# Performance work log

Measured on AMD Instinct MI355X. Metric: run time of the kernel, lower is better.

The kernel has to match this reference:

```python
import jax, jax.numpy as jnp
import numpy as np

B, C_IN, C_OUT = 16, 96, 192
N_IN, N_OUT, K = 16384, 4096, 16
SIGMA, MAX_ORD = 0.05, 2
M = 2 * MAX_ORD + 1  # basis size: 1 + cos/sin up to max_ord
BN_EPS = 1e-5


def _build_graph(rng):
    # random vertex layout; out vertices are a subset of in vertices
    vin = rng.standard_normal((N_IN, 2)).astype(np.float32)
    vout = vin[rng.choice(N_IN, N_OUT, replace=False)]
    idx = np.empty((N_OUT, K), np.int64)
    for s in range(0, N_OUT, 1024):  # chunked exact k-NN
        d = ((vout[s:s + 1024, None, :] - vin[None, :, :]) ** 2).sum(-1)
        idx[s:s + 1024] = np.argpartition(d, K, axis=1)[:, :K]
    rel = vin[idx] - vout[:, None, :]            # [N_out, K, 2]
    r2 = (rel ** 2).sum(-1)
    theta = np.arctan2(rel[..., 1], rel[..., 0])
    gauss = np.exp(-r2 / (2.0 * SIGMA ** 2))
    harm = [np.ones_like(theta)]
    for m in range(1, MAX_ORD + 1):
        harm += [np.cos(m * theta), np.sin(m * theta)]
    basis = (gauss[..., None] * np.stack(harm, -1)).astype(np.float32)  # [N_out, K, M]
    return idx, basis


def setup_inputs() -> dict:
    rng = np.random.default_rng(0)
    idx, basis = _build_graph(rng)
    key = jax.random.key(0)
    k0, k1, k2 = jax.random.split(key, 3)
    return {
        "x": jax.random.normal(k0, (B, C_IN, N_IN), jnp.float32),
        "idx": jnp.asarray(idx),
        "basis": jnp.asarray(basis),
        "conv_w": jax.random.normal(k1, (C_OUT, C_IN, M), jnp.float32) * 0.02,
        "conv_b": jnp.zeros((C_OUT,), jnp.float32),
        "pool_w": jax.random.normal(k2, (C_OUT, C_IN), jnp.float32) * 0.02,
        "pool_b": jnp.zeros((C_OUT,), jnp.float32),
        "gamma": jnp.ones((C_OUT,), jnp.float32),
        "beta": jnp.zeros((C_OUT,), jnp.float32),
    }


def reference(x, idx, basis, conv_w, conv_b, pool_w, pool_b, gamma, beta):
    # irregular k-NN gather: [B, C_in, N_out, K]
    neigh = x[:, :, idx]
    # identity path: AvgPool over k neighbors + 1x1 conv
    pooled = neigh.mean(axis=-1)                                   # [B, C_in, N_out]
    identity = jnp.einsum('oc,bcn->bon', pool_w, pooled) + pool_b[:, None]
    # ConvV2: project neighbors onto gaussian-harmonic basis, contract with weights
    feat = jnp.einsum('bcnk,nkm->bcnm', neigh, basis)              # [B, C_in, N_out, M]
    out = jnp.einsum('ocm,bcnm->bon', conv_w, feat) + conv_b[:, None]
    # BatchNorm1d (training-mode batch stats over B and N)
    mean = out.mean(axis=(0, 2), keepdims=True)
    var = out.var(axis=(0, 2), keepdims=True)
    out = (out - mean) * jax.lax.rsqrt(var + BN_EPS) * gamma[:, None] + beta[:, None]
    return out + identity
```

## Files before the change

kernel.cpp:

```cpp
#include <hip/hip_runtime.h>

typedef __attribute__((ext_vector_type(8))) short s16x8;
typedef __attribute__((ext_vector_type(4))) float f32x4;

constexpr int cB = 16, cCIN = 96, cCOUT = 192, cNIN = 16384, cNOUT = 4096;
constexpr float cEPS = 1e-5f;

constexpr size_t OFF_XT     = 0;
constexpr size_t OFF_CONVB  = 0;
constexpr size_t OFF_IDENTB = 25165824;
constexpr size_t OFF_FEATA  = 50331648;
constexpr size_t OFF_WB     = 125829120;
constexpr size_t OFF_SS     = 126050304;
constexpr size_t OFF_S1     = 126051840;
constexpr size_t OFF_S2     = 127624704;

__device__ inline unsigned bf16_rne(float f) {
    unsigned u = __builtin_bit_cast(unsigned, f);
    return (u + 0x7fffu + ((u >> 16) & 1u)) >> 16;
}
__device__ inline float bf16_f(unsigned short h) {
    unsigned u = ((unsigned)h) << 16;
    return __builtin_bit_cast(float, u);
}

__launch_bounds__(256)
__global__ void k_tr(const float* __restrict__ x, unsigned* __restrict__ xto) {
    __shared__ float s[96 * 133];
    const int b = blockIdx.y, j0 = blockIdx.x * 128, t = threadIdx.x;
    const float* xb = x + (size_t)b * 96 * 16384 + j0;
    for (int q = t; q < 3072; q += 256) {
        int c = q >> 5, j4 = (q & 31) * 4;
        float4 v = *(const float4*)(xb + (size_t)c * 16384 + j4);
        s[c * 133 + j4 + 0] = v.x;
        s[c * 133 + j4 + 1] = v.y;
        s[c * 133 + j4 + 2] = v.z;
        s[c * 133 + j4 + 3] = v.w;
    }
    __syncthreads();
    for (int q = t; q < 6144; q += 256) {
        int cp = q % 48, jj = q / 48;
        float f0 = s[(2 * cp) * 133 + jj];
        float f1 = s[(2 * cp + 1) * 133 + jj];
        unsigned pr = bf16_rne(f0) | (bf16_rne(f1) << 16);
        xto[(size_t)(b * 16384 + j0 + jj) * 48 + cp] = pr;
    }
}

__global__ void k_pack(const float* __restrict__ cw, const float* __restrict__ pw,
                       unsigned short* __restrict__ wB) {
    int e = blockIdx.x * 256 + threadIdx.x;
    if (e >= 110592) return;
    int r = e & 7, l = (e >> 3) & 63;
    int ts = e >> 9;
    int s = ts % 18, ot = ts / 18;
    int o = ot * 16 + (l & 15);
    int ko = s * 32 + ((l >> 4) << 3) + r;
    float v;
    if (ko < 480) { int m = ko / 96, c = ko % 96; v = cw[(o * 96 + c) * 5 + m]; }
    else          { int c = ko - 480;             v = pw[o * 96 + c]; }
    wB[e] = (unsigned short)bf16_rne(v);
}

__launch_bounds__(192)
__global__ void k_feat(const unsigned short* __restrict__ xt,
                       const int* __restrict__ idx,
                       const float* __restrict__ basis,
                       unsigned short* __restrict__ featA) {
    __shared__ float s_bas[16 * 97];
    __shared__ int s_idx[256];
    const int t = threadIdx.x, b = blockIdx.y, n0 = blockIdx.x * 16;

    for (int i = t; i < 256; i += 192)
        s_idx[i] = idx[n0 * 16 + i];
    for (int i = t; i < 16 * 96; i += 192) {
        int nl = i / 96, km = i % 96, k = km / 6, m = km % 6;
        float v = (m < 5) ? basis[((size_t)(n0 + nl) * 16 + k) * 5 + m] : 0.0625f;
        s_bas[nl * 97 + km] = v;
    }
    __syncthreads();

    const int c8 = t >> 4, nl = t & 15;
    float fm[6][8];
#pragma unroll
    for (int m = 0; m < 6; ++m)
#pragma unroll
        for (int j = 0; j < 8; ++j) fm[m][j] = 0.f;

    const size_t xbase = (size_t)b * 16384;
#pragma unroll 4
    for (int k = 0; k < 16; ++k) {
        int j = s_idx[nl * 16 + k];
        s16x8 v = *(const s16x8*)(xt + (xbase + j) * 96 + c8 * 8);
        float gf[8];
#pragma unroll
        for (int q = 0; q < 8; ++q) gf[q] = bf16_f((unsigned short)v[q]);
#pragma unroll
        for (int m = 0; m < 6; ++m) {
            float bv = s_bas[nl * 97 + k * 6 + m];
#pragma unroll
            for (int q = 0; q < 8; ++q) fm[m][q] = fmaf(gf[q], bv, fm[m][q]);
        }
    }

    const int tile = b * 256 + blockIdx.x;
    const int fl = nl + ((c8 & 3) << 4);
#pragma unroll
    for (int m = 0; m < 6; ++m) {
        int s = 3 * m + (c8 >> 2);
        uint4 o;
        o.x = bf16_rne(fm[m][0]) | (bf16_rne(fm[m][1]) << 16);
        o.y = bf16_rne(fm[m][2]) | (bf16_rne(fm[m][3]) << 16);
        o.z = bf16_rne(fm[m][4]) | (bf16_rne(fm[m][5]) << 16);
        o.w = bf16_rne(fm[m][6]) | (bf16_rne(fm[m][7]) << 16);
        *(uint4*)(featA + ((size_t)(tile * 18 + s) * 64 + fl) * 8) = o;
    }
}

__launch_bounds__(256)
__global__ void k_gemm(const unsigned short* __restrict__ featA,
                       const unsigned short* __restrict__ wB,
                       unsigned short* __restrict__ convb,
                       unsigned short* __restrict__ identb,
                       float* __restrict__ s1g,
                       float* __restrict__ s2g) {
    __shared__ __align__(16) unsigned short s_c[192 * 72];
    const int t = threadIdx.x;
    const int w = t >> 6, lane = t & 63;
    const int wr = w & 1, wc = w >> 1;
    const int bid = blockIdx.x;
    const int tile0 = bid * 4 + wr * 2;
    const s16x8* A  = (const s16x8*)featA;
    const s16x8* Bw = (const s16x8*)wB;

    f32x4 accC[2][6], accI[2][6];
    const f32x4 z = {0.f, 0.f, 0.f, 0.f};
#pragma unroll
    for (int rt = 0; rt < 2; ++rt)
#pragma unroll
        for (int j = 0; j < 6; ++j) { accC[rt][j] = z; accI[rt][j] = z; }

    for (int s = 0; s < 15; ++s) {
        s16x8 a0 = A[(size_t)(tile0 * 18 + s) * 64 + lane];
        s16x8 a1 = A[(size_t)((tile0 + 1) * 18 + s) * 64 + lane];
#pragma unroll
        for (int j = 0; j < 6; ++j) {
            s16x8 bf = Bw[(size_t)((wc * 6 + j) * 18 + s) * 64 + lane];
            accC[0][j] = __builtin_amdgcn_mfma_f32_16x16x32_bf16(a0, bf, accC[0][j], 0, 0, 0);
            accC[1][j] = __builtin_amdgcn_mfma_f32_16x16x32_bf16(a1, bf, accC[1][j], 0, 0, 0);
        }
    }
#pragma unroll
    for (int s = 15; s < 18; ++s) {
        s16x8 a0 = A[(size_t)(tile0 * 18 + s) * 64 + lane];
        s16x8 a1 = A[(size_t)((tile0 + 1) * 18 + s) * 64 + lane];
#pragma unroll
        for (int j = 0; j < 6; ++j) {
            s16x8 bf = Bw[(size_t)((wc * 6 + j) * 18 + s) * 64 + lane];
            accI[0][j] = __builtin_amdgcn_mfma_f32_16x16x32_bf16(a0, bf, accI[0][j], 0, 0, 0);
            accI[1][j] = __builtin_amdgcn_mfma_f32_16x16x32_bf16(a1, bf, accI[1][j], 0, 0, 0);
        }
    }

    const int col_l = lane & 15, rg = (lane >> 4) * 4;
    const int b  = (bid * 64) >> 12;
    const int n0 = (bid * 64) & 4095;

#pragma unroll
    for (int j = 0; j < 6; ++j) {
        float s1 = 0.f, s2 = 0.f;
#pragma unroll
        for (int rt = 0; rt < 2; ++rt)
#pragma unroll
            for (int r = 0; r < 4; ++r) {
                float v = accC[rt][j][r];
                s1 += v;
                s2 = fmaf(v, v, s2);
            }
        s1 += __shfl_xor(s1, 16); s2 += __shfl_xor(s2, 16);
        s1 += __shfl_xor(s1, 32); s2 += __shfl_xor(s2, 32);
        if (lane < 16) {
            int o = (wc * 6 + j) * 16 + lane;
            s1g[(size_t)o * 2048 + bid * 2 + wr] = s1;
            s2g[(size_t)o * 2048 + bid * 2 + wr] = s2;
        }
    }

#pragma unroll
    for (int rt = 0; rt < 2; ++rt) {
        int lr = (wr * 2 + rt) * 16 + rg;
#pragma unroll
        for (int j = 0; j < 6; ++j) {
            int o = (wc * 6 + j) * 16 + col_l;
#pragma unroll
            for (int r = 0; r < 4; ++r)
                s_c[o * 72 + lr + r] = (unsigned short)bf16_rne(accC[rt][j][r]);
        }
    }
    __syncthreads();
    for (int u = t; u < 1536; u += 256) {
        int o = u >> 3, part = u & 7;
        uint4 v = *(const uint4*)(&s_c[o * 72 + part * 8]);
        *(uint4*)(convb + ((size_t)(b * 192 + o)) * 4096 + n0 + part * 8) = v;
    }
    __syncthreads();
#pragma unroll
    for (int rt = 0; rt < 2; ++rt) {
        int lr = (wr * 2 + rt) * 16 + rg;
#pragma unroll
        for (int j = 0; j < 6; ++j) {
            int o = (wc * 6 + j) * 16 + col_l;
#pragma unroll
            for (int r = 0; r < 4; ++r)
                s_c[o * 72 + lr + r] = (unsigned short)bf16_rne(accI[rt][j][r]);
        }
    }
    __syncthreads();
    for (int u = t; u < 1536; u += 256) {
        int o = u >> 3, part = u & 7;
        uint4 v = *(const uint4*)(&s_c[o * 72 + part * 8]);
        *(uint4*)(identb + ((size_t)(b * 192 + o)) * 4096 + n0 + part * 8) = v;
    }
}

__launch_bounds__(256)
__global__ void k_ss(const float* __restrict__ s1g, const float* __restrict__ s2g,
                     const float* __restrict__ gamma, const float* __restrict__ beta,
                     const float* __restrict__ pool_b, float* __restrict__ ss) {
    int o = blockIdx.x, t = threadIdx.x;
    float s1 = 0.f, s2 = 0.f;
    for (int i = t; i < 2048; i += 256) {
        s1 += s1g[(size_t)o * 2048 + i];
        s2 += s2g[(size_t)o * 2048 + i];
    }
#pragma unroll
    for (int off = 32; off; off >>= 1) {
        s1 += __shfl_down(s1, off);
        s2 += __shfl_down(s2, off);
    }
    __shared__ float w1[4], w2[4];
    int lane = t & 63, wid = t >> 6;
    if (lane == 0) { w1[wid] = s1; w2[wid] = s2; }
    __syncthreads();
    if (t == 0) {
        float S1 = w1[0] + w1[1] + w1[2] + w1[3];
        float S2 = w2[0] + w2[1] + w2[2] + w2[3];
        float inv  = 1.0f / (cB * cNOUT);
        float mean = S1 * inv;
        float var  = S2 * inv - mean * mean;
        float scale = gamma[o] * rsqrtf(var + cEPS);
        ss[o]         = scale;
        ss[cCOUT + o] = beta[o] - mean * scale + pool_b[o];
    }
}

__launch_bounds__(256)
__global__ void k_final(const unsigned short* __restrict__ convb,
                        const unsigned short* __restrict__ identb,
                        const float* __restrict__ ss,
                        float* __restrict__ out) {
    size_t i = ((size_t)blockIdx.x * 256 + threadIdx.x) * 8;
    int o = (int)((i >> 12) % cCOUT);
    uint4 cv = *(const uint4*)(convb + i);
    uint4 dv = *(const uint4*)(identb + i);
    const unsigned short* ch = (const unsigned short*)&cv;
    const unsigned short* dh = (const unsigned short*)&dv;
    float sc = ss[o], sh = ss[cCOUT + o];
    float r[8];
#pragma unroll
    for (int j = 0; j < 8; ++j)
        r[j] = fmaf(bf16_f(ch[j]), sc, sh + bf16_f(dh[j]));
    *(float4*)(out + i)     = *(float4*)&r[0];
    *(float4*)(out + i + 4) = *(float4*)&r[4];
}

extern "C" void kernel_launch(void* const* d_in, const int* in_sizes, int n_in,
                              void* d_out, int out_size, void* d_ws, size_t ws_size,
                              hipStream_t stream) {
    const float* x      = (const float*)d_in[0];
    const int*   idx    = (const int*)d_in[1];
    const float* basis  = (const float*)d_in[2];
    const float* conv_w = (const float*)d_in[3];
    const float* pool_w = (const float*)d_in[5];
    const float* pool_b = (const float*)d_in[6];
    const float* gamma  = (const float*)d_in[7];
    const float* beta   = (const float*)d_in[8];
    float* out = (float*)d_out;

    char* wsb = (char*)d_ws;
    unsigned short* xt     = (unsigned short*)(wsb + OFF_XT);
    unsigned short* convb  = (unsigned short*)(wsb + OFF_CONVB);
    unsigned short* identb = (unsigned short*)(wsb + OFF_IDENTB);
    unsigned short* featA  = (unsigned short*)(wsb + OFF_FEATA);
    unsigned short* wB     = (unsigned short*)(wsb + OFF_WB);
    float*          ss     = (float*)(wsb + OFF_SS);
    float*          s1g    = (float*)(wsb + OFF_S1);
    float*          s2g    = (float*)(wsb + OFF_S2);

    k_tr   <<<dim3(cNIN / 128, cB), 256, 0, stream>>>(x, (unsigned*)xt);
    k_pack <<<(110592 + 255) / 256, 256, 0, stream>>>(conv_w, pool_w, wB);
    k_feat <<<dim3(cNOUT / 16, cB), 192, 0, stream>>>(xt, idx, basis, featA);
    k_gemm <<<(cB * cNOUT) / 64, 256, 0, stream>>>(featA, wB, convb, identb, s1g, s2g);
    k_ss   <<<cCOUT, 256, 0, stream>>>(s1g, s2g, gamma, beta, pool_b, ss);
    k_final<<<(size_t)cB * cCOUT * cNOUT / 2048, 256, 0, stream>>>(convb, identb, ss, out);
}
```

Measured before the change: 145.5 us.

## Widen transpose stores, XCD-remap feat blocks, split GEMM accumulators, prefetch A

The transpose kernel now packs four channels per thread and writes 8-byte stores instead of 4-byte ones. The gather kernel uses a 1D grid whose block index is remapped so each XCD handles two whole batches, keeping that batch's x slice in one L2. The GEMM kernel computes the identity-path accumulators only after the conv results are stored, cutting live registers so it can run with launch_bounds(256,3). Its main loop also software-prefetches the next A fragment. The prefetch reads one step past the conv K-range, which stays in bounds, and the later identity pass reloads A from memory.

```diff
diff --git a/kernel.cpp b/kernel.cpp
--- a/kernel.cpp
+++ b/kernel.cpp
@@ -38,12 +38,16 @@
         s[c * 133 + j4 + 3] = v.w;
     }
     __syncthreads();
-    for (int q = t; q < 6144; q += 256) {
-        int cp = q % 48, jj = q / 48;
-        float f0 = s[(2 * cp) * 133 + jj];
-        float f1 = s[(2 * cp + 1) * 133 + jj];
-        unsigned pr = bf16_rne(f0) | (bf16_rne(f1) << 16);
-        xto[(size_t)(b * 16384 + j0 + jj) * 48 + cp] = pr;
+    for (int q = t; q < 3072; q += 256) {
+        int cp2 = q % 24, jj = q / 24;
+        float f0 = s[(4 * cp2 + 0) * 133 + jj];
+        float f1 = s[(4 * cp2 + 1) * 133 + jj];
+        float f2 = s[(4 * cp2 + 2) * 133 + jj];
+        float f3 = s[(4 * cp2 + 3) * 133 + jj];
+        uint2 pr;
+        pr.x = bf16_rne(f0) | (bf16_rne(f1) << 16);
+        pr.y = bf16_rne(f2) | (bf16_rne(f3) << 16);
+        *(uint2*)(xto + (size_t)(b * 16384 + j0 + jj) * 48 + cp2 * 2) = pr;
     }
 }
 
@@ -69,7 +73,12 @@
                        unsigned short* __restrict__ featA) {
     __shared__ float s_bas[16 * 97];
     __shared__ int s_idx[256];
-    const int t = threadIdx.x, b = blockIdx.y, n0 = blockIdx.x * 16;
+    const int t = threadIdx.x;
+    const int wg = blockIdx.x;
+    const int xcd = wg & 7, slot = wg >> 3;
+    const int b  = xcd * 2 + (slot >> 8);
+    const int nt = slot & 255;
+    const int n0 = nt * 16;
 
     for (int i = t; i < 256; i += 192)
         s_idx[i] = idx[n0 * 16 + i];
@@ -103,7 +112,7 @@
         }
     }
 
-    const int tile = b * 256 + blockIdx.x;
+    const int tile = b * 256 + nt;
     const int fl = nl + ((c8 & 3) << 4);
 #pragma unroll
     for (int m = 0; m < 6; ++m) {
@@ -117,7 +126,7 @@
     }
 }
 
-__launch_bounds__(256)
+__launch_bounds__(256, 3)
 __global__ void k_gemm(const unsigned short* __restrict__ featA,
                        const unsigned short* __restrict__ wB,
                        unsigned short* __restrict__ convb,
@@ -133,33 +142,25 @@
     const s16x8* A  = (const s16x8*)featA;
     const s16x8* Bw = (const s16x8*)wB;
 
-    f32x4 accC[2][6], accI[2][6];
     const f32x4 z = {0.f, 0.f, 0.f, 0.f};
+    f32x4 accC[2][6];
 #pragma unroll
     for (int rt = 0; rt < 2; ++rt)
 #pragma unroll
-        for (int j = 0; j < 6; ++j) { accC[rt][j] = z; accI[rt][j] = z; }
-
+        for (int j = 0; j < 6; ++j) accC[rt][j] = z;
+
+    s16x8 a0 = A[(size_t)(tile0 * 18 + 0) * 64 + lane];
+    s16x8 a1 = A[(size_t)((tile0 + 1) * 18 + 0) * 64 + lane];
     for (int s = 0; s < 15; ++s) {
-        s16x8 a0 = A[(size_t)(tile0 * 18 + s) * 64 + lane];
-        s16x8 a1 = A[(size_t)((tile0 + 1) * 18 + s) * 64 + lane];
+        s16x8 na0 = A[(size_t)(tile0 * 18 + s + 1) * 64 + lane];
+        s16x8 na1 = A[(size_t)((tile0 + 1) * 18 + s + 1) * 64 + lane];
 #pragma unroll
         for (int j = 0; j < 6; ++j) {
             s16x8 bf = Bw[(size_t)((wc * 6 + j) * 18 + s) * 64 + lane];
             accC[0][j] = __builtin_amdgcn_mfma_f32_16x16x32_bf16(a0, bf, accC[0][j], 0, 0, 0);
             accC[1][j] = __builtin_amdgcn_mfma_f32_16x16x32_bf16(a1, bf, accC[1][j], 0, 0, 0);
         }
-    }
-#pragma unroll
-    for (int s = 15; s < 18; ++s) {
-        s16x8 a0 = A[(size_t)(tile0 * 18 + s) * 64 + lane];
-        s16x8 a1 = A[(size_t)((tile0 + 1) * 18 + s) * 64 + lane];
-#pragma unroll
-        for (int j = 0; j < 6; ++j) {
-            s16x8 bf = Bw[(size_t)((wc * 6 + j) * 18 + s) * 64 + lane];
-            accI[0][j] = __builtin_amdgcn_mfma_f32_16x16x32_bf16(a0, bf, accI[0][j], 0, 0, 0);
-            accI[1][j] = __builtin_amdgcn_mfma_f32_16x16x32_bf16(a1, bf, accI[1][j], 0, 0, 0);
-        }
+        a0 = na0; a1 = na1;
     }
 
     const int col_l = lane & 15, rg = (lane >> 4) * 4;
@@ -204,6 +205,24 @@
         *(uint4*)(convb + ((size_t)(b * 192 + o)) * 4096 + n0 + part * 8) = v;
     }
     __syncthreads();
+
+    f32x4 accI[2][6];
+#pragma unroll
+    for (int rt = 0; rt < 2; ++rt)
+#pragma unroll
+        for (int j = 0; j < 6; ++j) accI[rt][j] = z;
+#pragma unroll
+    for (int s = 15; s < 18; ++s) {
+        s16x8 b0 = A[(size_t)(tile0 * 18 + s) * 64 + lane];
+        s16x8 b1 = A[(size_t)((tile0 + 1) * 18 + s) * 64 + lane];
+#pragma unroll
+        for (int j = 0; j < 6; ++j) {
+            s16x8 bf = Bw[(size_t)((wc * 6 + j) * 18 + s) * 64 + lane];
+            accI[0][j] = __builtin_amdgcn_mfma_f32_16x16x32_bf16(b0, bf, accI[0][j], 0, 0, 0);
+            accI[1][j] = __builtin_amdgcn_mfma_f32_16x16x32_bf16(b1, bf, accI[1][j], 0, 0, 0);
+        }
+    }
+
 #pragma unroll
     for (int rt = 0; rt < 2; ++rt) {
         int lr = (wr * 2 + rt) * 16 + rg;
@@ -299,7 +318,7 @@
 
     k_tr   <<<dim3(cNIN / 128, cB), 256, 0, stream>>>(x, (unsigned*)xt);
     k_pack <<<(110592 + 255) / 256, 256, 0, stream>>>(conv_w, pool_w, wB);
-    k_feat <<<dim3(cNOUT / 16, cB), 192, 0, stream>>>(xt, idx, basis, featA);
+    k_feat <<<4096, 192, 0, stream>>>(xt, idx, basis, featA);
     k_gemm <<<(cB * cNOUT) / 64, 256, 0, stream>>>(featA, wB, convb, identb, s1g, s2g);
     k_ss   <<<cCOUT, 256, 0, stream>>>(s1g, s2g, gamma, beta, pool_b, ss);
     k_final<<<(size_t)cB * cCOUT * cNOUT / 2048, 256, 0, stream>>>(convb, identb, ss, out);
```

New measurement: 134.9 us. -7.3%, faster.
